# Kernel tuning notes

Measured on AMD Instinct MI355X. Metric: run time of the kernel, lower is better.

## Reference

```python
import jax, jax.numpy as jnp
import numpy as np

EPS = 1e-5
ALPHA = 0.1
STEPS = 2


def setup_inputs() -> dict:
    key = jax.random.key(0)
    k1, k2 = jax.random.split(key)
    B, S, n, d = 4, 4096, 4, 1024
    streams = jax.random.normal(k1, (B, S, n, d), dtype=jnp.float32)
    norm_scale = jnp.ones((n * d,), dtype=jnp.float32)
    # matches nn.init.normal_(std=0.01) on Linear weight, zero bias
    proj_w = jax.random.normal(k2, (3 * n * n, n * d), dtype=jnp.float32) * 0.01
    proj_b = jnp.zeros((3 * n * n,), dtype=jnp.float32)
    out_scale = jnp.ones((1,), dtype=jnp.float32) * 0.1
    return {"streams": streams, "norm_scale": norm_scale, "proj_w": proj_w,
            "proj_b": proj_b, "out_scale": out_scale}


def _cayley_iterative(H_raw, alpha=ALPHA, steps=STEPS):
    # Skew-symmetrize then fixed-point iterate toward Cayley transform.
    W = H_raw - jnp.swapaxes(H_raw, -2, -1)          # [B,S,n,n]
    I = jnp.eye(W.shape[-1], dtype=W.dtype)           # broadcasts over [B,S]
    Y = I + alpha * W
    for _ in range(steps):
        Y = I + (alpha / 2) * jnp.matmul(W, I + Y)
    return Y


def reference(streams, norm_scale, proj_w, proj_b, out_scale):
    B, S, n, d = streams.shape
    # --- _compute_matrices (shared by aggregate & distribute; same values) ---
    x = streams.reshape(B, S, n * d)
    rms = jnp.sqrt(jnp.mean(x * x, axis=-1, keepdims=True) + EPS)
    raw = (x / rms * norm_scale) @ proj_w.T + proj_b  # [B,S,3*n*n]
    raw = raw.reshape(B, S, 3, n, n)
    H_pre = jax.nn.softmax(raw[:, :, 0], axis=-1)     # row-stochastic
    H_post = jax.nn.softmax(raw[:, :, 1], axis=-2)    # column-stochastic
    H_res = _cayley_iterative(raw[:, :, 2])           # ~orthogonal [B,S,n,n]
    # --- aggregate: mix streams, mean over stream axis ---
    h_new = jnp.matmul(H_pre, streams).mean(axis=2)   # [B,S,d]
    # --- distribute: orthogonal residual + scaled broadcast of layer output ---
    residual = jnp.matmul(H_res, streams)             # [B,S,n,d]
    h_b = jnp.broadcast_to(h_new[:, :, None, :], streams.shape)
    output = jnp.matmul(H_post, h_b)                  # [B,S,n,d]
    return residual + out_scale * output
```

## Files before the change

### kernel.cpp

```cpp
#include <hip/hip_runtime.h>
#include <hip/hip_bf16.h>

#define T_PER_BLK 8
#define XS_ROW 2060
#define EPS_F 1e-5f

typedef __bf16 bf16x8 __attribute__((ext_vector_type(8)));
typedef float f32x4 __attribute__((ext_vector_type(4)));

static __device__ __forceinline__ unsigned int pack_bf16x2(float a, float b) {
    union { float f; unsigned int u; } ca, cb;
    ca.f = a; cb.f = b;
    unsigned int ua = (ca.u + 0x7fffu + ((ca.u >> 16) & 1u)) >> 16;
    unsigned int ub = (cb.u + 0x7fffu + ((cb.u >> 16) & 1u)) >> 16;
    return ua | (ub << 16);
}

__global__ void scale_weights(const float* __restrict__ w,
                              const float* __restrict__ ns,
                              unsigned int* __restrict__ wbf)
{
    const int i = (blockIdx.x * 256 + threadIdx.x) * 4;
    const float4 wv = *reinterpret_cast<const float4*>(w + i);
    const float4 nv = *reinterpret_cast<const float4*>(ns + (i & 4095));
    uint2 o;
    o.x = pack_bf16x2(wv.x * nv.x, wv.y * nv.y);
    o.y = pack_bf16x2(wv.z * nv.z, wv.w * nv.w);
    *reinterpret_cast<uint2*>(wbf + (i >> 1)) = o;
}

__global__ __launch_bounds__(512, 4)
void fused_stream_mix(const float* __restrict__ streams,
                      const unsigned short* __restrict__ wbf,
                      const float* __restrict__ proj_b,
                      const float* __restrict__ out_scale,
                      float* __restrict__ out)
{
    __shared__ unsigned int xs[T_PER_BLK][XS_ROW];
    __shared__ float red[8][3][8][16];

    const int tid  = threadIdx.x;
    const int wv   = tid >> 6;
    const int lane = tid & 63;
    const size_t tok0 = (size_t)blockIdx.x * T_PER_BLK;

    float invr;
    {
        const float* src = streams + (tok0 + wv) * 4096;
        float ssq = 0.f;
        #pragma unroll
        for (int j = 0; j < 16; ++j) {
            float4 v = *reinterpret_cast<const float4*>(src + j * 256 + lane * 4);
            ssq = fmaf(v.x, v.x, ssq); ssq = fmaf(v.y, v.y, ssq);
            ssq = fmaf(v.z, v.z, ssq); ssq = fmaf(v.w, v.w, ssq);
            const int di = j * 128 + lane * 2;
            xs[wv][di]     = pack_bf16x2(v.x, v.y);
            xs[wv][di + 1] = pack_bf16x2(v.z, v.w);
        }
        #pragma unroll
        for (int m = 32; m >= 1; m >>= 1) ssq += __shfl_xor(ssq, m, 64);
        invr = rsqrtf(ssq * (1.f / 4096.f) + EPS_F);
    }
    __syncthreads();

    {
        const int arow = lane & 7;
        const int koff = (lane >> 4) * 8;
        const int bcol = lane & 15;
        const int kbase = wv * 512;

        const unsigned int* xrow = &xs[arow][0];
        const unsigned short* wp = wbf + (size_t)bcol * 4096 + kbase + koff;

        f32x4 acc0 = {0.f, 0.f, 0.f, 0.f};
        f32x4 acc1 = acc0, acc2 = acc0;

        #pragma unroll 4
        for (int ks = 0; ks < 16; ++ks) {
            const int k = kbase + ks * 32 + koff;
            bf16x8 a  = *reinterpret_cast<const bf16x8*>(&xrow[k >> 1]);
            bf16x8 b0 = *reinterpret_cast<const bf16x8*>(wp + ks * 32);
            bf16x8 b1 = *reinterpret_cast<const bf16x8*>(wp + 16 * 4096 + ks * 32);
            bf16x8 b2 = *reinterpret_cast<const bf16x8*>(wp + 32 * 4096 + ks * 32);
            acc0 = __builtin_amdgcn_mfma_f32_16x16x32_bf16(a, b0, acc0, 0, 0, 0);
            acc1 = __builtin_amdgcn_mfma_f32_16x16x32_bf16(a, b1, acc1, 0, 0, 0);
            acc2 = __builtin_amdgcn_mfma_f32_16x16x32_bf16(a, b2, acc2, 0, 0, 0);
        }
        if (lane < 32) {
            const int col = lane & 15, rg = (lane >> 4) * 4;
            #pragma unroll
            for (int r = 0; r < 4; ++r) {
                red[wv][0][rg + r][col] = acc0[r];
                red[wv][1][rg + r][col] = acc1[r];
                red[wv][2][rg + r][col] = acc2[r];
            }
        }
    }
    __syncthreads();

    float Mr[16];
    {
        float raw[48];
        #pragma unroll
        for (int tile = 0; tile < 3; ++tile) {
            #pragma unroll
            for (int c4 = 0; c4 < 4; ++c4) {
                f32x4 s = {0.f, 0.f, 0.f, 0.f};
                #pragma unroll
                for (int kp = 0; kp < 8; ++kp) {
                    const f32x4 v = *reinterpret_cast<const f32x4*>(&red[kp][tile][wv][c4 * 4]);
                    s += v;
                }
                const float4 pb = *reinterpret_cast<const float4*>(&proj_b[tile * 16 + c4 * 4]);
                raw[tile*16 + c4*4 + 0] = s[0] * invr + pb.x;
                raw[tile*16 + c4*4 + 1] = s[1] * invr + pb.y;
                raw[tile*16 + c4*4 + 2] = s[2] * invr + pb.z;
                raw[tile*16 + c4*4 + 3] = s[3] * invr + pb.w;
            }
        }

        float c[4] = {0.f, 0.f, 0.f, 0.f};
        #pragma unroll
        for (int i = 0; i < 4; ++i) {
            const float a0 = raw[i*4+0], a1 = raw[i*4+1], a2 = raw[i*4+2], a3 = raw[i*4+3];
            const float m = fmaxf(fmaxf(a0, a1), fmaxf(a2, a3));
            const float e0 = expf(a0 - m), e1 = expf(a1 - m);
            const float e2 = expf(a2 - m), e3 = expf(a3 - m);
            const float inv = 1.f / (e0 + e1 + e2 + e3);
            c[0] = fmaf(e0, inv, c[0]); c[1] = fmaf(e1, inv, c[1]);
            c[2] = fmaf(e2, inv, c[2]); c[3] = fmaf(e3, inv, c[3]);
        }
        c[0] *= 0.25f; c[1] *= 0.25f; c[2] *= 0.25f; c[3] *= 0.25f;

        float rs[4] = {0.f, 0.f, 0.f, 0.f};
        #pragma unroll
        for (int j = 0; j < 4; ++j) {
            const float b0 = raw[16+j], b1 = raw[16+4+j], b2 = raw[16+8+j], b3 = raw[16+12+j];
            const float m = fmaxf(fmaxf(b0, b1), fmaxf(b2, b3));
            const float e0 = expf(b0 - m), e1 = expf(b1 - m);
            const float e2 = expf(b2 - m), e3 = expf(b3 - m);
            const float inv = 1.f / (e0 + e1 + e2 + e3);
            rs[0] = fmaf(e0, inv, rs[0]); rs[1] = fmaf(e1, inv, rs[1]);
            rs[2] = fmaf(e2, inv, rs[2]); rs[3] = fmaf(e3, inv, rs[3]);
        }

        float W[16], Y[16];
        #pragma unroll
        for (int i = 0; i < 4; ++i)
            #pragma unroll
            for (int j = 0; j < 4; ++j)
                W[i*4+j] = raw[32 + i*4+j] - raw[32 + j*4+i];
        #pragma unroll
        for (int i = 0; i < 16; ++i) Y[i] = 0.1f * W[i];
        Y[0] += 1.f; Y[5] += 1.f; Y[10] += 1.f; Y[15] += 1.f;
        #pragma unroll
        for (int it = 0; it < 2; ++it) {
            float T1[16];
            #pragma unroll
            for (int i = 0; i < 16; ++i) T1[i] = Y[i];
            T1[0] += 1.f; T1[5] += 1.f; T1[10] += 1.f; T1[15] += 1.f;
            float Yn[16];
            #pragma unroll
            for (int i = 0; i < 4; ++i)
                #pragma unroll
                for (int j = 0; j < 4; ++j) {
                    float s = W[i*4+0] * T1[0*4+j];
                    s = fmaf(W[i*4+1], T1[1*4+j], s);
                    s = fmaf(W[i*4+2], T1[2*4+j], s);
                    s = fmaf(W[i*4+3], T1[3*4+j], s);
                    Yn[i*4+j] = ((i == j) ? 1.f : 0.f) + 0.05f * s;
                }
            #pragma unroll
            for (int i = 0; i < 16; ++i) Y[i] = Yn[i];
        }

        const float os = out_scale[0];
        #pragma unroll
        for (int i = 0; i < 4; ++i)
            #pragma unroll
            for (int j = 0; j < 4; ++j)
                Mr[i*4+j] = Y[i*4+j] + os * rs[i] * c[j];
    }

    {
        float* dst = out + (tok0 + wv) * 4096;
        #pragma unroll
        for (int it = 0; it < 4; ++it) {
            const int cq = it * 64 + lane;
            float x[4][4];
            #pragma unroll
            for (int j = 0; j < 4; ++j) {
                const uint2 u = *reinterpret_cast<const uint2*>(&xs[wv][j * 512 + cq * 2]);
                x[j][0] = __uint_as_float(u.x << 16);
                x[j][1] = __uint_as_float(u.x & 0xffff0000u);
                x[j][2] = __uint_as_float(u.y << 16);
                x[j][3] = __uint_as_float(u.y & 0xffff0000u);
            }
            #pragma unroll
            for (int i = 0; i < 4; ++i) {
                float4 o;
                o.x = Mr[i*4+0]*x[0][0]; o.y = Mr[i*4+0]*x[0][1];
                o.z = Mr[i*4+0]*x[0][2]; o.w = Mr[i*4+0]*x[0][3];
                #pragma unroll
                for (int j = 1; j < 4; ++j) {
                    o.x = fmaf(Mr[i*4+j], x[j][0], o.x);
                    o.y = fmaf(Mr[i*4+j], x[j][1], o.y);
                    o.z = fmaf(Mr[i*4+j], x[j][2], o.z);
                    o.w = fmaf(Mr[i*4+j], x[j][3], o.w);
                }
                *reinterpret_cast<float4*>(dst + i * 1024 + cq * 4) = o;
            }
        }
    }
}

extern "C" void kernel_launch(void* const* d_in, const int* in_sizes, int n_in,
                              void* d_out, int out_size, void* d_ws, size_t ws_size,
                              hipStream_t stream) {
    const float* streams    = (const float*)d_in[0];
    const float* norm_scale = (const float*)d_in[1];
    const float* proj_w     = (const float*)d_in[2];
    const float* proj_b     = (const float*)d_in[3];
    const float* out_scale  = (const float*)d_in[4];
    float* outp = (float*)d_out;

    unsigned int* wbf = (unsigned int*)d_ws;

    scale_weights<<<dim3(192), 256, 0, stream>>>(proj_w, norm_scale, wbf);

    const int n_tok = in_sizes[0] / 4096;
    dim3 grid(n_tok / T_PER_BLK);
    fused_stream_mix<<<grid, 512, 0, stream>>>(streams,
                                               (const unsigned short*)wbf,
                                               proj_b, out_scale, outp);
}
```

Measured before the change: 168.9 us.

## Drop shared-memory token staging; keep bf16 stream copy in registers and reload A from global

Removes the 64KB shared xs buffer. Each wave now keeps its own token's bf16-packed data in 32 registers for the output mix, and the MFMA A operand is re-read as fp32 from global (likely L2-resident) and converted on the fly. This drops one __syncthreads and lowers LDS usage, which can raise occupancy. In exchange it adds register pressure and redundant global loads and conversions in the GEMM loop. The Cayley/softmax section is also restructured to reduce one tile at a time, shortening register live ranges.

```diff
diff --git a/kernel.cpp b/kernel.cpp
--- a/kernel.cpp
+++ b/kernel.cpp
@@ -2,7 +2,6 @@
 #include <hip/hip_bf16.h>
 
 #define T_PER_BLK 8
-#define XS_ROW 2060
 #define EPS_F 1e-5f
 
 typedef __bf16 bf16x8 __attribute__((ext_vector_type(8)));
@@ -15,6 +14,9 @@
     unsigned int ub = (cb.u + 0x7fffu + ((cb.u >> 16) & 1u)) >> 16;
     return ua | (ub << 16);
 }
+
+static __device__ __forceinline__ float bf_lo(unsigned int u) { return __uint_as_float(u << 16); }
+static __device__ __forceinline__ float bf_hi(unsigned int u) { return __uint_as_float(u & 0xffff0000u); }
 
 __global__ void scale_weights(const float* __restrict__ w,
                               const float* __restrict__ ns,
@@ -36,7 +38,6 @@
                       const float* __restrict__ out_scale,
                       float* __restrict__ out)
 {
-    __shared__ unsigned int xs[T_PER_BLK][XS_ROW];
     __shared__ float red[8][3][8][16];
 
     const int tid  = threadIdx.x;
@@ -44,6 +45,7 @@
     const int lane = tid & 63;
     const size_t tok0 = (size_t)blockIdx.x * T_PER_BLK;
 
+    unsigned int tv[32];
     float invr;
     {
         const float* src = streams + (tok0 + wv) * 4096;
@@ -53,15 +55,13 @@
             float4 v = *reinterpret_cast<const float4*>(src + j * 256 + lane * 4);
             ssq = fmaf(v.x, v.x, ssq); ssq = fmaf(v.y, v.y, ssq);
             ssq = fmaf(v.z, v.z, ssq); ssq = fmaf(v.w, v.w, ssq);
-            const int di = j * 128 + lane * 2;
-            xs[wv][di]     = pack_bf16x2(v.x, v.y);
-            xs[wv][di + 1] = pack_bf16x2(v.z, v.w);
+            tv[2 * j]     = pack_bf16x2(v.x, v.y);
+            tv[2 * j + 1] = pack_bf16x2(v.z, v.w);
         }
         #pragma unroll
         for (int m = 32; m >= 1; m >>= 1) ssq += __shfl_xor(ssq, m, 64);
         invr = rsqrtf(ssq * (1.f / 4096.f) + EPS_F);
     }
-    __syncthreads();
 
     {
         const int arow = lane & 7;
@@ -69,7 +69,7 @@
         const int bcol = lane & 15;
         const int kbase = wv * 512;
 
-        const unsigned int* xrow = &xs[arow][0];
+        const float* ap = streams + (tok0 + arow) * 4096 + kbase + koff;
         const unsigned short* wp = wbf + (size_t)bcol * 4096 + kbase + koff;
 
         f32x4 acc0 = {0.f, 0.f, 0.f, 0.f};
@@ -77,8 +77,11 @@
 
         #pragma unroll 4
         for (int ks = 0; ks < 16; ++ks) {
-            const int k = kbase + ks * 32 + koff;
-            bf16x8 a  = *reinterpret_cast<const bf16x8*>(&xrow[k >> 1]);
+            const float4 a0 = *reinterpret_cast<const float4*>(ap + ks * 32);
+            const float4 a1 = *reinterpret_cast<const float4*>(ap + ks * 32 + 4);
+            bf16x8 a;
+            a[0] = (__bf16)a0.x; a[1] = (__bf16)a0.y; a[2] = (__bf16)a0.z; a[3] = (__bf16)a0.w;
+            a[4] = (__bf16)a1.x; a[5] = (__bf16)a1.y; a[6] = (__bf16)a1.z; a[7] = (__bf16)a1.w;
             bf16x8 b0 = *reinterpret_cast<const bf16x8*>(wp + ks * 32);
             bf16x8 b1 = *reinterpret_cast<const bf16x8*>(wp + 16 * 4096 + ks * 32);
             bf16x8 b2 = *reinterpret_cast<const bf16x8*>(wp + 32 * 4096 + ks * 32);
@@ -100,56 +103,67 @@
 
     float Mr[16];
     {
-        float raw[48];
-        #pragma unroll
-        for (int tile = 0; tile < 3; ++tile) {
-            #pragma unroll
-            for (int c4 = 0; c4 < 4; ++c4) {
-                f32x4 s = {0.f, 0.f, 0.f, 0.f};
+        const float4 pb0 = *reinterpret_cast<const float4*>(&proj_b[0]);
+        #define REDUCE_TILE(tile, raw)                                             \
+            {                                                                      \
+                _Pragma("unroll")                                                  \
+                for (int c4 = 0; c4 < 4; ++c4) {                                   \
+                    f32x4 s = {0.f, 0.f, 0.f, 0.f};                                \
+                    _Pragma("unroll")                                              \
+                    for (int kp = 0; kp < 8; ++kp)                                 \
+                        s += *reinterpret_cast<const f32x4*>(&red[kp][tile][wv][c4 * 4]); \
+                    const float4 pb = *reinterpret_cast<const float4*>(&proj_b[tile * 16 + c4 * 4]); \
+                    raw[c4*4 + 0] = s[0] * invr + pb.x;                            \
+                    raw[c4*4 + 1] = s[1] * invr + pb.y;                            \
+                    raw[c4*4 + 2] = s[2] * invr + pb.z;                            \
+                    raw[c4*4 + 3] = s[3] * invr + pb.w;                            \
+                }                                                                  \
+            }
+        (void)pb0;
+
+        float c[4] = {0.f, 0.f, 0.f, 0.f};
+        {
+            float raw[16];
+            REDUCE_TILE(0, raw)
+            #pragma unroll
+            for (int i = 0; i < 4; ++i) {
+                const float a0 = raw[i*4+0], a1 = raw[i*4+1], a2 = raw[i*4+2], a3 = raw[i*4+3];
+                const float m = fmaxf(fmaxf(a0, a1), fmaxf(a2, a3));
+                const float e0 = expf(a0 - m), e1 = expf(a1 - m);
+                const float e2 = expf(a2 - m), e3 = expf(a3 - m);
+                const float inv = 1.f / (e0 + e1 + e2 + e3);
+                c[0] = fmaf(e0, inv, c[0]); c[1] = fmaf(e1, inv, c[1]);
+                c[2] = fmaf(e2, inv, c[2]); c[3] = fmaf(e3, inv, c[3]);
+            }
+            c[0] *= 0.25f; c[1] *= 0.25f; c[2] *= 0.25f; c[3] *= 0.25f;
+        }
+
+        float rs[4] = {0.f, 0.f, 0.f, 0.f};
+        {
+            float raw[16];
+            REDUCE_TILE(1, raw)
+            #pragma unroll
+            for (int j = 0; j < 4; ++j) {
+                const float b0 = raw[j], b1 = raw[4+j], b2 = raw[8+j], b3 = raw[12+j];
+                const float m = fmaxf(fmaxf(b0, b1), fmaxf(b2, b3));
+                const float e0 = expf(b0 - m), e1 = expf(b1 - m);
+                const float e2 = expf(b2 - m), e3 = expf(b3 - m);
+                const float inv = 1.f / (e0 + e1 + e2 + e3);
+                rs[0] = fmaf(e0, inv, rs[0]); rs[1] = fmaf(e1, inv, rs[1]);
+                rs[2] = fmaf(e2, inv, rs[2]); rs[3] = fmaf(e3, inv, rs[3]);
+            }
+        }
+
+        float W[16], Y[16];
+        {
+            float raw[16];
+            REDUCE_TILE(2, raw)
+            #pragma unroll
+            for (int i = 0; i < 4; ++i)
                 #pragma unroll
-                for (int kp = 0; kp < 8; ++kp) {
-                    const f32x4 v = *reinterpret_cast<const f32x4*>(&red[kp][tile][wv][c4 * 4]);
-                    s += v;
-                }
-                const float4 pb = *reinterpret_cast<const float4*>(&proj_b[tile * 16 + c4 * 4]);
-                raw[tile*16 + c4*4 + 0] = s[0] * invr + pb.x;
-                raw[tile*16 + c4*4 + 1] = s[1] * invr + pb.y;
-                raw[tile*16 + c4*4 + 2] = s[2] * invr + pb.z;
-                raw[tile*16 + c4*4 + 3] = s[3] * invr + pb.w;
-            }
-        }
-
-        float c[4] = {0.f, 0.f, 0.f, 0.f};
-        #pragma unroll
-        for (int i = 0; i < 4; ++i) {
-            const float a0 = raw[i*4+0], a1 = raw[i*4+1], a2 = raw[i*4+2], a3 = raw[i*4+3];
-            const float m = fmaxf(fmaxf(a0, a1), fmaxf(a2, a3));
-            const float e0 = expf(a0 - m), e1 = expf(a1 - m);
-            const float e2 = expf(a2 - m), e3 = expf(a3 - m);
-            const float inv = 1.f / (e0 + e1 + e2 + e3);
-            c[0] = fmaf(e0, inv, c[0]); c[1] = fmaf(e1, inv, c[1]);
-            c[2] = fmaf(e2, inv, c[2]); c[3] = fmaf(e3, inv, c[3]);
-        }
-        c[0] *= 0.25f; c[1] *= 0.25f; c[2] *= 0.25f; c[3] *= 0.25f;
-
-        float rs[4] = {0.f, 0.f, 0.f, 0.f};
-        #pragma unroll
-        for (int j = 0; j < 4; ++j) {
-            const float b0 = raw[16+j], b1 = raw[16+4+j], b2 = raw[16+8+j], b3 = raw[16+12+j];
-            const float m = fmaxf(fmaxf(b0, b1), fmaxf(b2, b3));
-            const float e0 = expf(b0 - m), e1 = expf(b1 - m);
-            const float e2 = expf(b2 - m), e3 = expf(b3 - m);
-            const float inv = 1.f / (e0 + e1 + e2 + e3);
-            rs[0] = fmaf(e0, inv, rs[0]); rs[1] = fmaf(e1, inv, rs[1]);
-            rs[2] = fmaf(e2, inv, rs[2]); rs[3] = fmaf(e3, inv, rs[3]);
-        }
-
-        float W[16], Y[16];
-        #pragma unroll
-        for (int i = 0; i < 4; ++i)
-            #pragma unroll
-            for (int j = 0; j < 4; ++j)
-                W[i*4+j] = raw[32 + i*4+j] - raw[32 + j*4+i];
+                for (int j = 0; j < 4; ++j)
+                    W[i*4+j] = raw[i*4+j] - raw[j*4+i];
+        }
         #pragma unroll
         for (int i = 0; i < 16; ++i) Y[i] = 0.1f * W[i];
         Y[0] += 1.f; Y[5] += 1.f; Y[10] += 1.f; Y[15] += 1.f;
@@ -180,21 +194,20 @@
             #pragma unroll
             for (int j = 0; j < 4; ++j)
                 Mr[i*4+j] = Y[i*4+j] + os * rs[i] * c[j];
+        #undef REDUCE_TILE
     }
 
     {
         float* dst = out + (tok0 + wv) * 4096;
         #pragma unroll
-        for (int it = 0; it < 4; ++it) {
-            const int cq = it * 64 + lane;
+        for (int jj = 0; jj < 4; ++jj) {
             float x[4][4];
             #pragma unroll
-            for (int j = 0; j < 4; ++j) {
-                const uint2 u = *reinterpret_cast<const uint2*>(&xs[wv][j * 512 + cq * 2]);
-                x[j][0] = __uint_as_float(u.x << 16);
-                x[j][1] = __uint_as_float(u.x & 0xffff0000u);
-                x[j][2] = __uint_as_float(u.y << 16);
-                x[j][3] = __uint_as_float(u.y & 0xffff0000u);
+            for (int r = 0; r < 4; ++r) {
+                const unsigned int u0 = tv[(r * 4 + jj) * 2];
+                const unsigned int u1 = tv[(r * 4 + jj) * 2 + 1];
+                x[r][0] = bf_lo(u0); x[r][1] = bf_hi(u0);
+                x[r][2] = bf_lo(u1); x[r][3] = bf_hi(u1);
             }
             #pragma unroll
             for (int i = 0; i < 4; ++i) {
@@ -202,13 +215,13 @@
                 o.x = Mr[i*4+0]*x[0][0]; o.y = Mr[i*4+0]*x[0][1];
                 o.z = Mr[i*4+0]*x[0][2]; o.w = Mr[i*4+0]*x[0][3];
                 #pragma unroll
-                for (int j = 1; j < 4; ++j) {
-                    o.x = fmaf(Mr[i*4+j], x[j][0], o.x);
-                    o.y = fmaf(Mr[i*4+j], x[j][1], o.y);
-                    o.z = fmaf(Mr[i*4+j], x[j][2], o.z);
-                    o.w = fmaf(Mr[i*4+j], x[j][3], o.w);
+                for (int r = 1; r < 4; ++r) {
+                    o.x = fmaf(Mr[i*4+r], x[r][0], o.x);
+                    o.y = fmaf(Mr[i*4+r], x[r][1], o.y);
+                    o.z = fmaf(Mr[i*4+r], x[r][2], o.z);
+                    o.w = fmaf(Mr[i*4+r], x[r][3], o.w);
                 }
-                *reinterpret_cast<float4*>(dst + i * 1024 + cq * 4) = o;
+                *reinterpret_cast<float4*>(dst + i * 1024 + jj * 256 + lane * 4) = o;
             }
         }
     }
```

New measurement: 262.2 us. +55.2%, slower.
